# Optimization experiments

Measured on AMD Instinct MI355X. Metric: run time of the kernel, lower is better.

Reference implementation:

```python
import jax, jax.numpy as jnp
import numpy as np

RADIUS = 0.5
NSAMPLE = 32
SAMPLING = 2
TRAD = 1
TSTRIDE = 1
TPAD = (1, 1)


def fps(xyz, m):
    """Furthest point sampling. xyz: [N,3] -> [m] int32 indices (starts at point 0,
    same heuristic as pointnet2_utils.furthest_point_sample)."""
    N = xyz.shape[0]
    def body(carry, _):
        dist, last = carry
        d = jnp.sum((xyz - xyz[last]) ** 2, axis=-1)
        dist = jnp.minimum(dist, d)
        nxt = jnp.argmax(dist).astype(jnp.int32)
        return (dist, nxt), last
    init = (jnp.full((N,), 1e10, xyz.dtype), jnp.zeros((), jnp.int32))
    _, idx = jax.lax.scan(body, init, None, length=m)
    return idx


def ball_query(anchor, neigh, radius, k):
    """anchor: [M,3], neigh: [N,3] -> [M,k] int32. First k in-radius indices,
    padded with the first found index (0 if none), matching pointnet2 ball_query."""
    N = neigh.shape[0]
    d2 = jnp.sum((anchor[:, None, :] - neigh[None, :, :]) ** 2, axis=-1)  # [M,N]
    cand = jnp.where(d2 < radius * radius, jnp.arange(N, dtype=jnp.int32), N)
    cand = jnp.sort(cand, axis=-1)[:, :k]  # first k valid indices, N = invalid
    first = cand[:, :1]
    first = jnp.where(first == N, 0, first)
    return jnp.where(cand == N, first, cand)


def pst_forward(xyzs, features, Ws0, Ws1, Wt):
    B, L, N, _ = xyzs.shape
    M = N // SAMPLING
    fx = [xyzs[:, t] for t in range(L)]            # each [B,N,3]
    ff = [features[:, t] for t in range(L)]        # each [B,C,N]
    # replicate temporal padding
    for _ in range(TPAD[0]):
        fx = [fx[0]] + fx
        ff = [ff[0]] + ff
    for _ in range(TPAD[1]):
        fx = fx + [fx[-1]]
        ff = ff + [ff[-1]]

    fps_b = jax.vmap(fps, in_axes=(0, None))
    bq_b = jax.vmap(ball_query, in_axes=(0, 0, None, None))
    gather_xyz = jax.vmap(lambda pts, idx: pts[idx])            # [N,3],[M,K]->[M,K,3]
    gather_feat = jax.vmap(lambda f, idx: f[:, idx])            # [C,N],[M,K]->[C,M,K]

    new_xyzs, new_feats = [], []
    for t in range(TRAD, len(fx) - TRAD, TSTRIDE):
        aidx = fps_b(fx[t], M)                                  # [B,M]
        anchor = jnp.take_along_axis(fx[t], aidx[..., None], axis=1)  # [B,M,3]
        st = 0.0
        for j, i in enumerate(range(t - TRAD, t + TRAD + 1)):
            idx = bq_b(anchor, fx[i], RADIUS, NSAMPLE)          # [B,M,K]
            ng = gather_xyz(fx[i], idx)                         # [B,M,K,3]
            disp = ng - anchor[:, :, None, :]                   # [B,M,K,3]
            fg = gather_feat(ff[i], idx)                        # [B,C,M,K]
            sf = jnp.concatenate([jnp.transpose(disp, (0, 3, 1, 2)), fg], axis=1)  # [B,3+C,M,K]
            h = jax.nn.relu(jnp.einsum('oc,bcmk->bomk', Ws0, sf))
            h = jax.nn.relu(jnp.einsum('oc,bcmk->bomk', Ws1, h))
            h = jnp.max(h, axis=-1)                             # [B,C1,M]
            st = st + jax.nn.relu(jnp.einsum('oc,bcm->bom', Wt[j], h))
        new_xyzs.append(anchor)
        new_feats.append(st)
    return jnp.stack(new_xyzs, axis=1), jnp.stack(new_feats, axis=1)


def setup_inputs() -> dict:
    key = jax.random.key(0)
    k1, k2, k3, k4, k5 = jax.random.split(key, 5)
    B, L, N, C = 4, 8, 4096, 3
    return {
        'xyzs': jax.random.normal(k1, (B, L, N, 3), jnp.float32),
        'features': jax.random.normal(k2, (B, L, C, N), jnp.float32),
        'Ws0': jax.random.normal(k3, (64, 3 + C), jnp.float32) * 0.1,
        'Ws1': jax.random.normal(k4, (128, 64), jnp.float32) * 0.05,
        'Wt': jax.random.normal(k5, (3, 256, 128), jnp.float32) * 0.05,
    }


def reference(xyzs, features, Ws0, Ws1, Wt):
    return pst_forward(xyzs, features, Ws0, Ws1, Wt)
```

## Files before the change

kernel.cpp:

```cpp
#include <hip/hip_runtime.h>
#include <hip/hip_bf16.h>
#include <cstddef>

#define B_  4
#define N_  4096
#define M_  2048
#define K_  32

__device__ __forceinline__ float sq3_rn(float dx, float dy, float dz) {
    return __fadd_rn(__fadd_rn(__fmul_rn(dx, dx), __fmul_rn(dy, dy)), __fmul_rn(dz, dz));
}

__global__ __launch_bounds__(512) void fps_kernel(
    const float* __restrict__ xyzs,
    float* __restrict__ out_xyz)
{
    const int blk = blockIdx.x;
    const int tid = threadIdx.x;
    const float* fr = xyzs + (size_t)blk * (N_ * 3);
    float* ox = out_xyz + (size_t)blk * (M_ * 3);

    __shared__ float sx[N_], sy[N_], sz[N_];
    __shared__ unsigned long long sred[2][8];

    float px[8], py[8], pz[8], dist[8];
#pragma unroll
    for (int u = 0; u < 8; ++u) {
        const int p = u * 512 + tid;
        const float x = fr[p*3+0], y = fr[p*3+1], z = fr[p*3+2];
        px[u] = x; py[u] = y; pz[u] = z; dist[u] = 1e10f;
        sx[p] = x; sy[p] = y; sz[p] = z;
    }
    __syncthreads();

    const int lane = tid & 63, wave = tid >> 6;
    int last = 0;
    for (int it = 0; it < M_; ++it) {
        const float lx = sx[last], ly = sy[last], lz = sz[last];
        if (tid == 0) { ox[it*3+0] = lx; ox[it*3+1] = ly; ox[it*3+2] = lz; }

        unsigned long long best = 0ull;
#pragma unroll
        for (int u = 0; u < 8; ++u) {
            const float d = sq3_rn(px[u]-lx, py[u]-ly, pz[u]-lz);
            const float nd = fminf(dist[u], d);
            dist[u] = nd;
            const unsigned long long pk =
                ((unsigned long long)__float_as_uint(nd) << 32) |
                (unsigned)(~(u * 512 + tid));
            best = pk > best ? pk : best;
        }
#pragma unroll
        for (int off = 32; off; off >>= 1) {
            const unsigned long long o = __shfl_xor(best, off);
            best = o > best ? o : best;
        }
        if (lane == 0) sred[it & 1][wave] = best;
        __syncthreads();
        const unsigned long long* sr = sred[it & 1];
        unsigned long long b = sr[0];
#pragma unroll
        for (int w = 1; w < 8; ++w) { const unsigned long long o = sr[w]; b = o > b ? o : b; }
        last = (int)((~(unsigned)b) & (N_ - 1));
    }
}

__global__ __launch_bounds__(256, 2) void mlp_kernel(
    const float* __restrict__ xyzs,
    const float* __restrict__ feats,
    const float* __restrict__ Ws0,
    const float* __restrict__ Ws1,
    const float* __restrict__ Wt,
    const float* __restrict__ anchors,
    float* __restrict__ out_feat)
{
    const int blk = blockIdx.x;
    const int mb  = blk & 511;
    const int bt  = blk >> 9;
    const int b = bt >> 3, t = bt & 7;
    const int tid = threadIdx.x;
    const int lane = tid & 63, wa = tid >> 6;

    __shared__ float ws1T[64 * 128];
    __shared__ float h1T[4][64][32];
    __shared__ float hmax[4][128];
    __shared__ float w0s[64][8];
    __shared__ float anc[4][3];
    __shared__ unsigned short sbidx[4][32];

    for (int i = tid; i < 384; i += 256) w0s[i / 6][i % 6] = Ws0[i];
    {
        const float4* wp4 = (const float4*)Ws1;
#pragma unroll
        for (int u = 0; u < 8; ++u) {
            const int f4 = u * 256 + tid;
            const float4 v = wp4[f4];
            const int oc = f4 >> 4;
            const int k0 = (f4 & 15) * 4;
            const int base = (oc >> 3) * 4 + ((oc >> 2) & 1) * 64 + (oc & 3);
            ws1T[(k0 + 0) * 128 + base] = v.x;
            ws1T[(k0 + 1) * 128 + base] = v.y;
            ws1T[(k0 + 2) * 128 + base] = v.z;
            ws1T[(k0 + 3) * 128 + base] = v.w;
        }
    }
    if (tid < 12) anc[tid / 3][tid % 3] =
        anchors[((size_t)bt * M_ + mb * 4 + tid / 3) * 3 + tid % 3];
    __syncthreads();

    const int p  = tid & 127;
    const int oh = tid >> 7;
    const int pa = p >> 5, nb = p & 31;
    const int og = lane >> 2;
    const int qg = lane & 3;

    float st0 = 0.f, st1 = 0.f, st2 = 0.f, st3 = 0.f;

    for (int j = 0; j < 3; ++j) {
        int fi = t + j - 1; fi = fi < 0 ? 0 : (fi > 7 ? 7 : fi);
        const float* fr = xyzs + (size_t)(b * 8 + fi) * (N_ * 3);

        {
            const float ax = anc[wa][0], ay = anc[wa][1], az = anc[wa][2];
            int cnt = 0, first = 0;
            for (int c = 0; c < 64; ++c) {
                const int n = c * 64 + lane;
                const float d2 = sq3_rn(fr[n*3+0]-ax, fr[n*3+1]-ay, fr[n*3+2]-az);
                const bool hit = d2 < 0.25f;
                const unsigned long long mask = __ballot(hit);
                if (mask) {
                    if (cnt == 0) first = c * 64 + __builtin_ctzll(mask);
                    if (hit) {
                        const int pos = cnt + (int)__popcll(mask & ((1ull << lane) - 1ull));
                        if (pos < K_) sbidx[wa][pos] = (unsigned short)n;
                    }
                    cnt += (int)__popcll(mask);
                    if (cnt >= K_) break;
                }
            }
            if (lane < K_ && lane >= cnt) sbidx[wa][lane] = (unsigned short)(cnt ? first : 0);
        }
        __syncthreads();

        {
            const int n = sbidx[pa][nb];
            const float* nx = xyzs + ((size_t)(b*8 + fi) * N_ + n) * 3;
            const float X = nx[0], Y = nx[1], Z = nx[2];
            const float* fp = feats + (size_t)(b*8 + fi) * (3 * N_) + n;
            const float f0 = fp[0], f1 = fp[N_], f2 = fp[2 * N_];
            const float s0 = X - anc[pa][0], s1 = Y - anc[pa][1], s2 = Z - anc[pa][2];
#pragma unroll
            for (int o4 = 0; o4 < 8; ++o4) {
#pragma unroll
                for (int oo = 0; oo < 4; ++oo) {
                    const int o = oh * 32 + o4 * 4 + oo;
                    const float4 A  = *(const float4*)&w0s[o][0];
                    const float4 Bv = *(const float4*)&w0s[o][4];
                    const float r = A.x*s0 + A.y*s1 + A.z*s2 + A.w*f0 + Bv.x*f1 + Bv.y*f2;
                    h1T[pa][o][nb] = fmaxf(r, 0.f);
                }
            }
        }
        __syncthreads();

        {
            float4 acc[8][2];
#pragma unroll
            for (int i = 0; i < 8; ++i) {
                acc[i][0] = make_float4(0.f, 0.f, 0.f, 0.f);
                acc[i][1] = make_float4(0.f, 0.f, 0.f, 0.f);
            }
            const float* wbase = ws1T + og * 4;
            const float* hbase = &h1T[wa][0][qg * 8];
#define FMA8(ocr, ws) \
    acc[ocr][0].x += ws*h0.x; acc[ocr][0].y += ws*h0.y; acc[ocr][0].z += ws*h0.z; acc[ocr][0].w += ws*h0.w; \
    acc[ocr][1].x += ws*h1.x; acc[ocr][1].y += ws*h1.y; acc[ocr][1].z += ws*h1.z; acc[ocr][1].w += ws*h1.w;
#pragma unroll 4
            for (int k = 0; k < 64; ++k) {
                const float4 h0 = *(const float4*)(hbase + k * 32);
                const float4 h1 = *(const float4*)(hbase + k * 32 + 4);
                const float4 w0 = *(const float4*)(wbase + k * 128);
                const float4 w1 = *(const float4*)(wbase + k * 128 + 64);
                FMA8(0, w0.x) FMA8(1, w0.y) FMA8(2, w0.z) FMA8(3, w0.w)
                FMA8(4, w1.x) FMA8(5, w1.y) FMA8(6, w1.z) FMA8(7, w1.w)
            }
#undef FMA8
#pragma unroll
            for (int ocr = 0; ocr < 8; ++ocr) {
                float m = fmaxf(
                    fmaxf(fmaxf(acc[ocr][0].x, acc[ocr][0].y), fmaxf(acc[ocr][0].z, acc[ocr][0].w)),
                    fmaxf(fmaxf(acc[ocr][1].x, acc[ocr][1].y), fmaxf(acc[ocr][1].z, acc[ocr][1].w)));
                m = fmaxf(m, __shfl_xor(m, 1));
                m = fmaxf(m, __shfl_xor(m, 2));
                if (qg == 0) hmax[wa][og * 8 + ocr] = fmaxf(m, 0.f);
            }
        }
        __syncthreads();

        {
            const float4* wr = (const float4*)(Wt + ((size_t)j << 15) + ((size_t)tid << 7));
            float c0 = 0.f, c1 = 0.f, c2 = 0.f, c3 = 0.f;
#pragma unroll 8
            for (int k4 = 0; k4 < 32; ++k4) {
                const float4 w  = wr[k4];
                const float4 m0 = *(const float4*)&hmax[0][k4 * 4];
                const float4 m1 = *(const float4*)&hmax[1][k4 * 4];
                const float4 m2 = *(const float4*)&hmax[2][k4 * 4];
                const float4 m3 = *(const float4*)&hmax[3][k4 * 4];
                c0 += w.x*m0.x + w.y*m0.y + w.z*m0.z + w.w*m0.w;
                c1 += w.x*m1.x + w.y*m1.y + w.z*m1.z + w.w*m1.w;
                c2 += w.x*m2.x + w.y*m2.y + w.z*m2.z + w.w*m2.w;
                c3 += w.x*m3.x + w.y*m3.y + w.z*m3.z + w.w*m3.w;
            }
            st0 += fmaxf(c0, 0.f);
            st1 += fmaxf(c1, 0.f);
            st2 += fmaxf(c2, 0.f);
            st3 += fmaxf(c3, 0.f);
        }
    }

    *(float4*)(out_feat + ((size_t)bt * 256 + tid) * M_ + mb * 4) =
        make_float4(st0, st1, st2, st3);
}

extern "C" void kernel_launch(void* const* d_in, const int* in_sizes, int n_in,
                              void* d_out, int out_size, void* d_ws, size_t ws_size,
                              hipStream_t stream) {
    const float* xyzs  = (const float*)d_in[0];
    const float* feats = (const float*)d_in[1];
    const float* Ws0   = (const float*)d_in[2];
    const float* Ws1   = (const float*)d_in[3];
    const float* Wt    = (const float*)d_in[4];

    float* out_xyz  = (float*)d_out;
    float* out_feat = out_xyz + (size_t)B_ * 8 * M_ * 3;

    (void)d_ws; (void)ws_size;

    fps_kernel<<<B_ * 8, 512, 0, stream>>>(xyzs, out_xyz);
    mlp_kernel<<<B_ * 8 * (M_ / 4), 256, 0, stream>>>(xyzs, feats, Ws0, Ws1, Wt,
                                                      out_xyz, out_feat);
}
```

Measured before the change: 4.413 ms.

## Use split-bf16 MFMA for the second MLP layer and remove block barriers

The second pointwise MLP layer moves from scalar FP32 FMAs to bf16 MFMA instructions. Weights and activations are each split into hi/lo bf16 parts and three products are summed to approximate FP32 accuracy. Each wave now owns one anchor end to end, which removes the per-stage __syncthreads and the shared h1 buffer. The temporal Wt projection is rearranged per wave and staged through shared memory for a coalesced store. The FPS kernel defers its output writes to the end instead of issuing one write per iteration. Occupancy is raised to 3 blocks per CU. The split-bf16 scheme risks small numerical differences and spends extra MFMA work to recover precision.

After: 9.282 ms. 2.1x slower.

```diff
diff --git a/kernel.cpp b/kernel.cpp
--- a/kernel.cpp
+++ b/kernel.cpp
@@ -1,5 +1,4 @@
 #include <hip/hip_runtime.h>
-#include <hip/hip_bf16.h>
 #include <cstddef>
 
 #define B_  4
@@ -7,8 +6,19 @@
 #define M_  2048
 #define K_  32
 
+typedef short bf16x8 __attribute__((ext_vector_type(8)));
+typedef float f32x4  __attribute__((ext_vector_type(4)));
+
 __device__ __forceinline__ float sq3_rn(float dx, float dy, float dz) {
     return __fadd_rn(__fadd_rn(__fmul_rn(dx, dx), __fmul_rn(dy, dy)), __fmul_rn(dz, dz));
+}
+
+__device__ __forceinline__ unsigned short f2bf(float f) {
+    unsigned u = __float_as_uint(f);
+    return (unsigned short)((u + 0x7FFFu + ((u >> 16) & 1u)) >> 16);
+}
+__device__ __forceinline__ float bf2f(unsigned short h) {
+    return __uint_as_float(((unsigned)h) << 16);
 }
 
 __global__ __launch_bounds__(512) void fps_kernel(
@@ -24,48 +34,63 @@
     __shared__ unsigned long long sred[2][8];
 
     float px[8], py[8], pz[8], dist[8];
+    unsigned ids[8];
 #pragma unroll
     for (int u = 0; u < 8; ++u) {
         const int p = u * 512 + tid;
         const float x = fr[p*3+0], y = fr[p*3+1], z = fr[p*3+2];
         px[u] = x; py[u] = y; pz[u] = z; dist[u] = 1e10f;
+        ids[u] = ~(unsigned)p;
         sx[p] = x; sy[p] = y; sz[p] = z;
     }
     __syncthreads();
 
     const int lane = tid & 63, wave = tid >> 6;
     int last = 0;
-    for (int it = 0; it < M_; ++it) {
-        const float lx = sx[last], ly = sy[last], lz = sz[last];
-        if (tid == 0) { ox[it*3+0] = lx; ox[it*3+1] = ly; ox[it*3+2] = lz; }
-
-        unsigned long long best = 0ull;
-#pragma unroll
-        for (int u = 0; u < 8; ++u) {
-            const float d = sq3_rn(px[u]-lx, py[u]-ly, pz[u]-lz);
-            const float nd = fminf(dist[u], d);
-            dist[u] = nd;
-            const unsigned long long pk =
-                ((unsigned long long)__float_as_uint(nd) << 32) |
-                (unsigned)(~(u * 512 + tid));
-            best = pk > best ? pk : best;
-        }
-#pragma unroll
-        for (int off = 32; off; off >>= 1) {
-            const unsigned long long o = __shfl_xor(best, off);
-            best = o > best ? o : best;
-        }
-        if (lane == 0) sred[it & 1][wave] = best;
-        __syncthreads();
-        const unsigned long long* sr = sred[it & 1];
-        unsigned long long b = sr[0];
-#pragma unroll
-        for (int w = 1; w < 8; ++w) { const unsigned long long o = sr[w]; b = o > b ? o : b; }
-        last = (int)((~(unsigned)b) & (N_ - 1));
-    }
-}
-
-__global__ __launch_bounds__(256, 2) void mlp_kernel(
+    int widx[4];
+#pragma unroll
+    for (int s = 0; s < 4; ++s) {
+        for (int ii = 0; ii < 512; ++ii) {
+            if (ii == tid) widx[s] = last;
+            const float lx = sx[last], ly = sy[last], lz = sz[last];
+
+            unsigned long long best = 0ull;
+#pragma unroll
+            for (int u = 0; u < 8; ++u) {
+                const float d = sq3_rn(px[u]-lx, py[u]-ly, pz[u]-lz);
+                const float nd = fminf(dist[u], d);
+                dist[u] = nd;
+                const unsigned long long pk =
+                    ((unsigned long long)__float_as_uint(nd) << 32) | ids[u];
+                best = pk > best ? pk : best;
+            }
+#pragma unroll
+            for (int off = 32; off; off >>= 1) {
+                const unsigned long long o = __shfl_xor(best, off);
+                best = o > best ? o : best;
+            }
+            if (lane == 0) sred[ii & 1][wave] = best;
+            __syncthreads();
+            const unsigned long long* sr = sred[ii & 1];
+            unsigned long long b0 = sr[0] > sr[1] ? sr[0] : sr[1];
+            unsigned long long b1 = sr[2] > sr[3] ? sr[2] : sr[3];
+            unsigned long long b2 = sr[4] > sr[5] ? sr[4] : sr[5];
+            unsigned long long b3 = sr[6] > sr[7] ? sr[6] : sr[7];
+            b0 = b0 > b1 ? b0 : b1;
+            b2 = b2 > b3 ? b2 : b3;
+            b0 = b0 > b2 ? b0 : b2;
+            last = (int)((~(unsigned)b0) & (N_ - 1));
+        }
+    }
+#pragma unroll
+    for (int s = 0; s < 4; ++s) {
+        const int it = s * 512 + tid;
+        const int w = widx[s];
+        ox[it*3+0] = sx[w]; ox[it*3+1] = sy[w]; ox[it*3+2] = sz[w];
+    }
+}
+
+__global__ __launch_bounds__(256, 3) void mlp_kernel(
     const float* __restrict__ xyzs,
     const float* __restrict__ feats,
     const float* __restrict__ Ws0,
@@ -80,13 +105,14 @@
     const int b = bt >> 3, t = bt & 7;
     const int tid = threadIdx.x;
     const int lane = tid & 63, wa = tid >> 6;
-
-    __shared__ float ws1T[64 * 128];
-    __shared__ float h1T[4][64][32];
-    __shared__ float hmax[4][128];
+    const int lm = lane & 15, lg = lane >> 4;
+
+    __shared__ unsigned short ws1s[2][128 * 64];
     __shared__ float w0s[64][8];
-    __shared__ float anc[4][3];
+    __shared__ float hmaxs[4][128];
+    __shared__ float ancs[4][3];
     __shared__ unsigned short sbidx[4][32];
+    float* stg = (float*)ws1s;
 
     for (int i = tid; i < 384; i += 256) w0s[i / 6][i % 6] = Ws0[i];
     {
@@ -97,23 +123,23 @@
             const float4 v = wp4[f4];
             const int oc = f4 >> 4;
             const int k0 = (f4 & 15) * 4;
-            const int base = (oc >> 3) * 4 + ((oc >> 2) & 1) * 64 + (oc & 3);
-            ws1T[(k0 + 0) * 128 + base] = v.x;
-            ws1T[(k0 + 1) * 128 + base] = v.y;
-            ws1T[(k0 + 2) * 128 + base] = v.z;
-            ws1T[(k0 + 3) * 128 + base] = v.w;
-        }
-    }
-    if (tid < 12) anc[tid / 3][tid % 3] =
+            const float vv[4] = {v.x, v.y, v.z, v.w};
+#pragma unroll
+            for (int c = 0; c < 4; ++c) {
+                const int k = k0 + c;
+                const int idx = oc * 64 + (((k >> 3) ^ (oc & 7)) << 3) + (k & 7);
+                const unsigned short hi = f2bf(vv[c]);
+                const unsigned short lo = f2bf(vv[c] - bf2f(hi));
+                ws1s[0][idx] = hi;
+                ws1s[1][idx] = lo;
+            }
+        }
+    }
+    if (tid < 12) ancs[tid / 3][tid % 3] =
         anchors[((size_t)bt * M_ + mb * 4 + tid / 3) * 3 + tid % 3];
     __syncthreads();
 
-    const int p  = tid & 127;
-    const int oh = tid >> 7;
-    const int pa = p >> 5, nb = p & 31;
-    const int og = lane >> 2;
-    const int qg = lane & 3;
-
+    const float ax = ancs[wa][0], ay = ancs[wa][1], az = ancs[wa][2];
     float st0 = 0.f, st1 = 0.f, st2 = 0.f, st3 = 0.f;
 
     for (int j = 0; j < 3; ++j) {
@@ -121,7 +147,6 @@
         const float* fr = xyzs + (size_t)(b * 8 + fi) * (N_ * 3);
 
         {
-            const float ax = anc[wa][0], ay = anc[wa][1], az = anc[wa][2];
             int cnt = 0, first = 0;
             for (int c = 0; c < 64; ++c) {
                 const int n = c * 64 + lane;
@@ -140,77 +165,101 @@
             }
             if (lane < K_ && lane >= cnt) sbidx[wa][lane] = (unsigned short)(cnt ? first : 0);
         }
-        __syncthreads();
-
+
+        bf16x8 bhi[2][2], blo[2][2];
         {
-            const int n = sbidx[pa][nb];
-            const float* nx = xyzs + ((size_t)(b*8 + fi) * N_ + n) * 3;
-            const float X = nx[0], Y = nx[1], Z = nx[2];
-            const float* fp = feats + (size_t)(b*8 + fi) * (3 * N_) + n;
-            const float f0 = fp[0], f1 = fp[N_], f2 = fp[2 * N_];
-            const float s0 = X - anc[pa][0], s1 = Y - anc[pa][1], s2 = Z - anc[pa][2];
-#pragma unroll
-            for (int o4 = 0; o4 < 8; ++o4) {
-#pragma unroll
-                for (int oo = 0; oo < 4; ++oo) {
-                    const int o = oh * 32 + o4 * 4 + oo;
+            const int n0 = sbidx[wa][lm];
+            const int n1 = sbidx[wa][16 + lm];
+            const float* nx0 = xyzs + ((size_t)(b*8 + fi) * N_ + n0) * 3;
+            const float* nx1 = xyzs + ((size_t)(b*8 + fi) * N_ + n1) * 3;
+            const float* fp  = feats + (size_t)(b*8 + fi) * (3 * N_);
+            const float s00 = nx0[0]-ax, s01 = nx0[1]-ay, s02 = nx0[2]-az;
+            const float s10 = nx1[0]-ax, s11 = nx1[1]-ay, s12 = nx1[2]-az;
+            const float f00 = fp[n0], f01 = fp[N_ + n0], f02 = fp[2*N_ + n0];
+            const float f10 = fp[n1], f11 = fp[N_ + n1], f12 = fp[2*N_ + n1];
+#pragma unroll
+            for (int ks = 0; ks < 2; ++ks) {
+#pragma unroll
+                for (int jj = 0; jj < 8; ++jj) {
+                    const int o = ks * 32 + lg * 8 + jj;
                     const float4 A  = *(const float4*)&w0s[o][0];
                     const float4 Bv = *(const float4*)&w0s[o][4];
-                    const float r = A.x*s0 + A.y*s1 + A.z*s2 + A.w*f0 + Bv.x*f1 + Bv.y*f2;
-                    h1T[pa][o][nb] = fmaxf(r, 0.f);
+                    const float r0 = fmaxf(A.x*s00 + A.y*s01 + A.z*s02 +
+                                           A.w*f00 + Bv.x*f01 + Bv.y*f02, 0.f);
+                    const float r1 = fmaxf(A.x*s10 + A.y*s11 + A.z*s12 +
+                                           A.w*f10 + Bv.x*f11 + Bv.y*f12, 0.f);
+                    const unsigned short h0 = f2bf(r0);
+                    const unsigned short h1 = f2bf(r1);
+                    bhi[0][ks][jj] = (short)h0;
+                    blo[0][ks][jj] = (short)f2bf(r0 - bf2f(h0));
+                    bhi[1][ks][jj] = (short)h1;
+                    blo[1][ks][jj] = (short)f2bf(r1 - bf2f(h1));
                 }
             }
         }
-        __syncthreads();
 
         {
-            float4 acc[8][2];
-#pragma unroll
-            for (int i = 0; i < 8; ++i) {
-                acc[i][0] = make_float4(0.f, 0.f, 0.f, 0.f);
-                acc[i][1] = make_float4(0.f, 0.f, 0.f, 0.f);
-            }
-            const float* wbase = ws1T + og * 4;
-            const float* hbase = &h1T[wa][0][qg * 8];
-#define FMA8(ocr, ws) \
-    acc[ocr][0].x += ws*h0.x; acc[ocr][0].y += ws*h0.y; acc[ocr][0].z += ws*h0.z; acc[ocr][0].w += ws*h0.w; \
-    acc[ocr][1].x += ws*h1.x; acc[ocr][1].y += ws*h1.y; acc[ocr][1].z += ws*h1.z; acc[ocr][1].w += ws*h1.w;
+            f32x4 acc[8][2];
+#pragma unroll
+            for (int mt = 0; mt < 8; ++mt) {
+                acc[mt][0] = (f32x4){0.f, 0.f, 0.f, 0.f};
+                acc[mt][1] = (f32x4){0.f, 0.f, 0.f, 0.f};
+            }
+#pragma unroll
+            for (int mt = 0; mt < 8; ++mt) {
+#pragma unroll
+                for (int ks = 0; ks < 2; ++ks) {
+                    const int oc = mt * 16 + lm;
+                    const int kb = ks * 32 + lg * 8;
+                    const int idx = oc * 64 + ((((kb >> 3) ^ (oc & 7))) << 3);
+                    const bf16x8 ahi = *(const bf16x8*)&ws1s[0][idx];
+                    const bf16x8 alo = *(const bf16x8*)&ws1s[1][idx];
+#pragma unroll
+                    for (int nt = 0; nt < 2; ++nt) {
+                        acc[mt][nt] = __builtin_amdgcn_mfma_f32_16x16x32_bf16(
+                            ahi, bhi[nt][ks], acc[mt][nt], 0, 0, 0);
+                        acc[mt][nt] = __builtin_amdgcn_mfma_f32_16x16x32_bf16(
+                            ahi, blo[nt][ks], acc[mt][nt], 0, 0, 0);
+                        acc[mt][nt] = __builtin_amdgcn_mfma_f32_16x16x32_bf16(
+                            alo, bhi[nt][ks], acc[mt][nt], 0, 0, 0);
+                    }
+                }
+            }
+#pragma unroll
+            for (int mt = 0; mt < 8; ++mt) {
+                float mr0 = fmaxf(acc[mt][0][0], acc[mt][1][0]);
+                float mr1 = fmaxf(acc[mt][0][1], acc[mt][1][1]);
+                float mr2 = fmaxf(acc[mt][0][2], acc[mt][1][2]);
+                float mr3 = fmaxf(acc[mt][0][3], acc[mt][1][3]);
+#pragma unroll
+                for (int off = 1; off < 16; off <<= 1) {
+                    mr0 = fmaxf(mr0, __shfl_xor(mr0, off));
+                    mr1 = fmaxf(mr1, __shfl_xor(mr1, off));
+                    mr2 = fmaxf(mr2, __shfl_xor(mr2, off));
+                    mr3 = fmaxf(mr3, __shfl_xor(mr3, off));
+                }
+                if (lm == 0)
+                    *(float4*)&hmaxs[wa][mt * 16 + lg * 4] =
+                        make_float4(fmaxf(mr0, 0.f), fmaxf(mr1, 0.f),
+                                    fmaxf(mr2, 0.f), fmaxf(mr3, 0.f));
+            }
+        }
+
+        {
+            const float4* wr = (const float4*)(Wt + ((size_t)j << 15) + ((size_t)lane << 9));
+            const float4* hm = (const float4*)&hmaxs[wa][0];
+            float c0 = 0.f, c1 = 0.f, c2 = 0.f, c3 = 0.f;
 #pragma unroll 4
-            for (int k = 0; k < 64; ++k) {
-                const float4 h0 = *(const float4*)(hbase + k * 32);
-                const float4 h1 = *(const float4*)(hbase + k * 32 + 4);
-                const float4 w0 = *(const float4*)(wbase + k * 128);
-                const float4 w1 = *(const float4*)(wbase + k * 128 + 64);
-                FMA8(0, w0.x) FMA8(1, w0.y) FMA8(2, w0.z) FMA8(3, w0.w)
-                FMA8(4, w1.x) FMA8(5, w1.y) FMA8(6, w1.z) FMA8(7, w1.w)
-            }
-#undef FMA8
-#pragma unroll
-            for (int ocr = 0; ocr < 8; ++ocr) {
-                float m = fmaxf(
-                    fmaxf(fmaxf(acc[ocr][0].x, acc[ocr][0].y), fmaxf(acc[ocr][0].z, acc[ocr][0].w)),
-                    fmaxf(fmaxf(acc[ocr][1].x, acc[ocr][1].y), fmaxf(acc[ocr][1].z, acc[ocr][1].w)));
-                m = fmaxf(m, __shfl_xor(m, 1));
-                m = fmaxf(m, __shfl_xor(m, 2));
-                if (qg == 0) hmax[wa][og * 8 + ocr] = fmaxf(m, 0.f);
-            }
-        }
-        __syncthreads();
-
-        {
-            const float4* wr = (const float4*)(Wt + ((size_t)j << 15) + ((size_t)tid << 7));
-            float c0 = 0.f, c1 = 0.f, c2 = 0.f, c3 = 0.f;
-#pragma unroll 8
             for (int k4 = 0; k4 < 32; ++k4) {
-                const float4 w  = wr[k4];
-                const float4 m0 = *(const float4*)&hmax[0][k4 * 4];
-                const float4 m1 = *(const float4*)&hmax[1][k4 * 4];
-                const float4 m2 = *(const float4*)&hmax[2][k4 * 4];
-                const float4 m3 = *(const float4*)&hmax[3][k4 * 4];
-                c0 += w.x*m0.x + w.y*m0.y + w.z*m0.z + w.w*m0.w;
-                c1 += w.x*m1.x + w.y*m1.y + w.z*m1.z + w.w*m1.w;
-                c2 += w.x*m2.x + w.y*m2.y + w.z*m2.z + w.w*m2.w;
-                c3 += w.x*m3.x + w.y*m3.y + w.z*m3.z + w.w*m3.w;
+                const float4 h  = hm[k4];
+                const float4 w0 = wr[k4];
+                const float4 w1 = wr[32 + k4];
+                const float4 w2 = wr[64 + k4];
+                const float4 w3 = wr[96 + k4];
+                c0 += w0.x*h.x + w0.y*h.y + w0.z*h.z + w0.w*h.w;
+                c1 += w1.x*h.x + w1.y*h.y + w1.z*h.z + w1.w*h.w;
+                c2 += w2.x*h.x + w2.y*h.y + w2.z*h.z + w2.w*h.w;
+                c3 += w3.x*h.x + w3.y*h.y + w3.z*h.z + w3.w*h.w;
             }
             st0 += fmaxf(c0, 0.f);
             st1 += fmaxf(c1, 0.f);
@@ -219,8 +268,20 @@
         }
     }
 
-    *(float4*)(out_feat + ((size_t)bt * 256 + tid) * M_ + mb * 4) =
-        make_float4(st0, st1, st2, st3);
+    __syncthreads();
+    stg[(lane * 4 + 0) * 6 + wa] = st0;
+    stg[(lane * 4 + 1) * 6 + wa] = st1;
+    stg[(lane * 4 + 2) * 6 + wa] = st2;
+    stg[(lane * 4 + 3) * 6 + wa] = st3;
+    __syncthreads();
+    {
+        float4 o;
+        o.x = stg[tid * 6 + 0];
+        o.y = stg[tid * 6 + 1];
+        o.z = stg[tid * 6 + 2];
+        o.w = stg[tid * 6 + 3];
+        *(float4*)(out_feat + ((size_t)bt * 256 + tid) * M_ + mb * 4) = o;
+    }
 }
 
 extern "C" void kernel_launch(void* const* d_in, const int* in_sizes, int n_in,
```
